# Kernel optimization log

Hardware: AMD Instinct MI355X
Metric: run time of the kernel (lower is better)

The kernel has to match this reference:

```python
import math
import jax, jax.numpy as jnp
import numpy as np

HEADS = 16
REL_WINDOW = 128


def setup_inputs() -> dict:
    key = jax.random.key(0)
    k1, k2, k3, k4, k5 = jax.random.split(key, 5)
    b, s, d = 2, 2048, 1024
    hd = d // HEADS          # 64
    R = 2 * REL_WINDOW + 1   # 257
    return {
        "x": jax.random.normal(k1, (b, s, d), dtype=jnp.float32),
        "Wqkv": jax.random.normal(k2, (3 * d, d), dtype=jnp.float32) * (1.0 / math.sqrt(d)),
        "bqkv": jax.random.normal(k3, (3 * d,), dtype=jnp.float32) * 0.02,
        "Wr": jax.random.normal(k4, (R, hd), dtype=jnp.float32) * (1.0 / math.sqrt(hd)),
        "br": jax.random.normal(k5, (R,), dtype=jnp.float32) * 0.02,
    }


def reference(x, Wqkv, bqkv, Wr, br):
    b, s, d = x.shape
    h = HEADS
    hd = d // h
    w = REL_WINDOW
    scale = math.sqrt(d / h)

    # qkv projection; torch view(b,s,h,3*hd) then chunk(3, dim=-1)
    qkv = (x @ Wqkv.T + bqkv).reshape(b, s, h, 3 * hd)
    q, k, v = jnp.split(qkv, 3, axis=-1)          # each [b,s,h,hd]
    q = q.transpose(0, 2, 1, 3)                   # [b,h,s,hd]
    k = k.transpose(0, 2, 1, 3)
    v = v.transpose(0, 2, 1, 3)

    # content scores
    content = jnp.einsum('bhik,bhjk->bhij', q, k) / scale  # [b,h,s,s]

    # relative position scores: project queries to R logits, gather per (i,j) offset
    idx = jnp.arange(s)
    offsets = jnp.clip(idx[None, :] - idx[:, None], -w, w) + w  # [s,s] in [0, 2w]
    rp = jnp.einsum('bhik,rk->bhir', q, Wr) + br               # [b,h,s,R]
    pos = jnp.take_along_axis(rp, jnp.broadcast_to(offsets, (b, h, s, s)), axis=-1)

    attn = jax.nn.softmax(content + pos, axis=-1)
    out = jnp.einsum('bhij,bhjk->bhik', attn, v)  # [b,h,s,hd]
    return out.transpose(0, 2, 1, 3).reshape(b, s, d)
```

## Files before the change

### kernel.cpp

```cpp
#include <hip/hip_runtime.h>

typedef short bfrag __attribute__((ext_vector_type(8)));
typedef float f32x4 __attribute__((ext_vector_type(4)));

#define MFMA16(a, b, c) __builtin_amdgcn_mfma_f32_16x16x32_bf16((a), (b), (c), 0, 0, 0)

#define SEQ   2048
#define DMOD  1024
#define NHEAD 16
#define HDIM  64
#define RSZ   257
#define RSTRIDE 260
#define RPADN 272
#define XN    (4096*1024)
#define WN    (3072*1024)
#define LOG2E 1.44269504f

__device__ __forceinline__ unsigned short f2bf(float f) {
  unsigned int u = __float_as_uint(f);
  u += 0x7FFFu + ((u >> 16) & 1u);
  return (unsigned short)(u >> 16);
}
__device__ __forceinline__ float bf2f(unsigned short u) {
  return __uint_as_float(((unsigned int)u) << 16);
}
__device__ __forceinline__ unsigned int pkbf(float a, float b) {
#if defined(__gfx950__)
  unsigned int r;
  asm("v_cvt_pk_bf16_f32 %0, %1, %2" : "=v"(r) : "v"(a), "v"(b));
  return r;
#else
  return (unsigned int)f2bf(a) | ((unsigned int)f2bf(b) << 16);
#endif
}
__device__ __forceinline__ float fexp2(float x) {
#if __has_builtin(__builtin_amdgcn_exp2f)
  return __builtin_amdgcn_exp2f(x);
#else
  return __expf(x * 0.69314718f);
#endif
}
__device__ __forceinline__ void gl2lds16(const void* g, void* l) {
  __builtin_amdgcn_global_load_lds(
      (__attribute__((address_space(1))) void*)(g),
      (__attribute__((address_space(3))) void*)(l), 16, 0, 0);
}

__global__ __launch_bounds__(256) void cast_all(const float* __restrict__ x,
                                                const float* __restrict__ Wqkv,
                                                const float* __restrict__ Wr,
                                                unsigned short* __restrict__ xb,
                                                unsigned short* __restrict__ wb,
                                                unsigned short* __restrict__ wrb) {
  int i = (blockIdx.x * 256 + threadIdx.x) * 4;
  if (i < XN) {
    float4 v = *(const float4*)(x + i);
    ushort4 o; o.x = f2bf(v.x); o.y = f2bf(v.y); o.z = f2bf(v.z); o.w = f2bf(v.w);
    *(ushort4*)(xb + i) = o;
  } else if (i < XN + WN) {
    int j = i - XN;
    float4 v = *(const float4*)(Wqkv + j);
    ushort4 o; o.x = f2bf(v.x); o.y = f2bf(v.y); o.z = f2bf(v.z); o.w = f2bf(v.w);
    *(ushort4*)(wb + j) = o;
  } else {
    int j = i - XN - WN;
    ushort4 o;
    unsigned short t[4];
#pragma unroll
    for (int k = 0; k < 4; ++k)
      t[k] = (j + k < RSZ * HDIM) ? f2bf(Wr[j + k]) : (unsigned short)0;
    o.x = t[0]; o.y = t[1]; o.z = t[2]; o.w = t[3];
    *(ushort4*)(wrb + j) = o;
  }
}

__global__ __launch_bounds__(256) void qkv_gemm(const unsigned short* __restrict__ xb,
                                                const unsigned short* __restrict__ wb,
                                                const float* __restrict__ bqkv,
                                                unsigned short* __restrict__ qb,
                                                unsigned short* __restrict__ kbuf,
                                                unsigned short* __restrict__ vtb) {
  __shared__ unsigned short SMEM[2 * 128 * 64];
  unsigned short* As = SMEM;
  unsigned short* Bs = SMEM + 128 * 64;
  unsigned short* Vtmp = SMEM;
  const int tid = threadIdx.x;
  const int m0 = blockIdx.y * 128, n0 = blockIdx.x * 128;
  const int wave = tid >> 6, lane = tid & 63;
  const int q4 = lane >> 4, l16 = lane & 15;
  const int wm = (wave & 1) * 64, wn = (wave >> 1) * 64;
  const int sw = l16 & 7;

  f32x4 acc[4][4];
#pragma unroll
  for (int rt = 0; rt < 4; ++rt)
#pragma unroll
    for (int ct = 0; ct < 4; ++ct) acc[rt][ct] = (f32x4){0.f, 0.f, 0.f, 0.f};

  for (int k0 = 0; k0 < DMOD; k0 += 64) {
#pragma unroll
    for (int it = 0; it < 4; ++it) {
      int ch = it * 256 + tid;
      int r = ch >> 3, cl = (ch & 7) ^ (r & 7);
      gl2lds16(xb + (size_t)(m0 + r) * DMOD + k0 + cl * 8, As + ch * 8);
      gl2lds16(wb + (size_t)(n0 + r) * DMOD + k0 + cl * 8, Bs + ch * 8);
    }
    __syncthreads();
#pragma unroll
    for (int ks = 0; ks < 2; ++ks) {
      bfrag af[4], bf[4];
#pragma unroll
      for (int rt = 0; rt < 4; ++rt)
        af[rt] = *(const bfrag*)(As + (wm + rt * 16 + l16) * 64 + ((ks * 4 + q4) ^ sw) * 8);
#pragma unroll
      for (int ct = 0; ct < 4; ++ct)
        bf[ct] = *(const bfrag*)(Bs + (wn + ct * 16 + l16) * 64 + ((ks * 4 + q4) ^ sw) * 8);
#pragma unroll
      for (int rt = 0; rt < 4; ++rt)
#pragma unroll
        for (int ct = 0; ct < 4; ++ct)
          acc[rt][ct] = MFMA16(bf[ct], af[rt], acc[rt][ct]);
    }
    __syncthreads();
  }

  const int batch = m0 >> 11;
  const int sbase = m0 & 2047;
  const int r3 = blockIdx.x % 3;
  const bool hasV = (r3 != 0);
  const int nv0 = n0 + ((r3 == 2) ? 64 : 0);

#pragma unroll
  for (int ct = 0; ct < 4; ++ct) {
    int ng = n0 + wn + ct * 16 + q4 * 4;
    int hh = ng / 192;
    int rem = ng - hh * 192;
    int t = rem >> 6, dd = rem & 63;
    float4 b4 = *(const float4*)(bqkv + ng);
    if (t < 2) {
      unsigned short* dst = (t == 0) ? qb : kbuf;
      size_t rowo = ((size_t)(batch * NHEAD + hh)) * SEQ + sbase;
#pragma unroll
      for (int rt = 0; rt < 4; ++rt) {
        int m = wm + rt * 16 + l16;
        uint2 pv;
        pv.x = pkbf(acc[rt][ct][0] + b4.x, acc[rt][ct][1] + b4.y);
        pv.y = pkbf(acc[rt][ct][2] + b4.z, acc[rt][ct][3] + b4.w);
        *(uint2*)(dst + (rowo + m) * HDIM + dd) = pv;
      }
    } else {
#pragma unroll
      for (int rt = 0; rt < 4; ++rt) {
        int m = wm + rt * 16 + l16;
        Vtmp[(dd + 0) * 136 + m] = f2bf(acc[rt][ct][0] + b4.x);
        Vtmp[(dd + 1) * 136 + m] = f2bf(acc[rt][ct][1] + b4.y);
        Vtmp[(dd + 2) * 136 + m] = f2bf(acc[rt][ct][2] + b4.z);
        Vtmp[(dd + 3) * 136 + m] = f2bf(acc[rt][ct][3] + b4.w);
      }
    }
  }

  if (hasV) {
    __syncthreads();
    const int hh = nv0 / 192;
    unsigned short* vdst = vtb + ((size_t)(batch * NHEAD + hh)) * HDIM * SEQ;
#pragma unroll
    for (int it = 0; it < 4; ++it) {
      int u = it * 256 + tid;
      int dd = u >> 4, mc = u & 15;
      bfrag val = *(const bfrag*)(Vtmp + dd * 136 + mc * 8);
      *(bfrag*)(vdst + (size_t)dd * SEQ + sbase + mc * 8) = val;
    }
  }
}

__global__ __launch_bounds__(256) void rp_gemm(const unsigned short* __restrict__ qb,
                                               const unsigned short* __restrict__ wrb,
                                               const float* __restrict__ br,
                                               unsigned short* __restrict__ rp16) {
  __shared__ unsigned short WrS[RPADN * HDIM];
  __shared__ unsigned short Qs[64 * HDIM];
  const int tid = threadIdx.x;
  const size_t row0 = (size_t)blockIdx.x * 64;

  for (int i = tid; i < RPADN * HDIM / 8; i += 256)
    *(uint4*)(&WrS[i * 8]) = *(const uint4*)(&wrb[i * 8]);
  for (int i = tid; i < 512; i += 256)
    *(uint4*)(&Qs[i * 8]) = *(const uint4*)(&qb[row0 * HDIM + i * 8]);
  __syncthreads();

  const int wave = tid >> 6, lane = tid & 63;
  const int q4 = lane >> 4, l16 = lane & 15;

  bfrag af0 = *(const bfrag*)(Qs + (wave * 16 + l16) * 64 + q4 * 8);
  bfrag af1 = *(const bfrag*)(Qs + (wave * 16 + l16) * 64 + 32 + q4 * 8);

  unsigned short* rrow = rp16 + (row0 + wave * 16 + l16) * RSTRIDE;
  const float br256 = br[256];

#pragma unroll 4
  for (int ct = 0; ct < 16; ++ct) {
    f32x4 acc = (f32x4){0.f, 0.f, 0.f, 0.f};
    bfrag w0 = *(const bfrag*)(WrS + (ct * 16 + l16) * 64 + q4 * 8);
    bfrag w1 = *(const bfrag*)(WrS + (ct * 16 + l16) * 64 + 32 + q4 * 8);
    acc = MFMA16(w0, af0, acc);
    acc = MFMA16(w1, af1, acc);
    int r = ct * 16 + q4 * 4;
    float4 b4 = *(const float4*)(br + r);
    uint2 pv;
    pv.x = pkbf((acc[0] + b4.x) * LOG2E, (acc[1] + b4.y) * LOG2E);
    pv.y = pkbf((acc[2] + b4.z) * LOG2E, (acc[3] + b4.w) * LOG2E);
    *(uint2*)(rrow + r) = pv;
  }
  {
    f32x4 acc = (f32x4){0.f, 0.f, 0.f, 0.f};
    bfrag w0 = *(const bfrag*)(WrS + (256 + l16) * 64 + q4 * 8);
    bfrag w1 = *(const bfrag*)(WrS + (256 + l16) * 64 + 32 + q4 * 8);
    acc = MFMA16(w0, af0, acc);
    acc = MFMA16(w1, af1, acc);
    if (q4 == 0)
      rrow[256] = f2bf((acc[0] + br256) * LOG2E);
  }
}

__global__ __launch_bounds__(256) void flash_attn(const unsigned short* __restrict__ qb,
                                                  const unsigned short* __restrict__ kbuf,
                                                  const unsigned short* __restrict__ vtb,
                                                  const unsigned short* __restrict__ rp16,
                                                  float* __restrict__ out) {
  __shared__ unsigned short Ks[64 * 64];
  __shared__ unsigned short Vs[64 * 64];
  __shared__ unsigned short Ps[64 * 64];

  const int tid = threadIdx.x;
  const int i0 = blockIdx.x * 64;
  const int bh = blockIdx.y;
  const int wave = tid >> 6, lane = tid & 63;
  const int q4 = lane >> 4, l16 = lane & 15;
  const int sw = l16 & 7;
  const float SC = 0.125f * LOG2E;

  const int rloc = wave * 16 + l16;
  const int ig = i0 + rloc;
  const unsigned short* qrow = qb + ((size_t)bh * SEQ + ig) * HDIM;
  bfrag qf0 = *(const bfrag*)(qrow + q4 * 8);
  bfrag qf1 = *(const bfrag*)(qrow + 32 + q4 * 8);

  const unsigned short* rpbase = rp16 + ((size_t)bh * SEQ + ig) * RSTRIDE;
  const float rpL = bf2f(rpbase[0]);
  const float rpR = bf2f(rpbase[256]);

  float m_s = -3.0e38f, l_s = 0.f;
  f32x4 oacc[4];
#pragma unroll
  for (int ct = 0; ct < 4; ++ct) oacc[ct] = (f32x4){0.f, 0.f, 0.f, 0.f};

  const unsigned short* kbase = kbuf + (size_t)bh * SEQ * HDIM;
  const unsigned short* vbase = vtb + (size_t)bh * HDIM * SEQ;

  for (int jt = 0; jt < 32; ++jt) {
    const int j0 = jt * 64;
#pragma unroll
    for (int it = 0; it < 2; ++it) {
      int ch = it * 256 + tid;
      int r = ch >> 3, cl = (ch & 7) ^ (r & 7);
      gl2lds16(kbase + (size_t)(j0 + r) * HDIM + cl * 8, Ks + ch * 8);
      gl2lds16(vbase + (size_t)r * SEQ + j0 + cl * 8, Vs + ch * 8);
    }
    __syncthreads();

    f32x4 sacc[4];
#pragma unroll
    for (int ct = 0; ct < 4; ++ct) {
      sacc[ct] = (f32x4){0.f, 0.f, 0.f, 0.f};
      bfrag k0f = *(const bfrag*)(Ks + (ct * 16 + l16) * 64 + (q4 ^ sw) * 8);
      bfrag k1f = *(const bfrag*)(Ks + (ct * 16 + l16) * 64 + ((4 + q4) ^ sw) * 8);
      sacc[ct] = MFMA16(k0f, qf0, sacc[ct]);
      sacc[ct] = MFMA16(k1f, qf1, sacc[ct]);
    }

    float p[4][4];
    const int dj = j0 - i0;
    if (dj >= 191) {
#pragma unroll
      for (int ct = 0; ct < 4; ++ct)
#pragma unroll
        for (int reg = 0; reg < 4; ++reg)
          p[ct][reg] = sacc[ct][reg] * SC + rpR;
    } else if (dj <= -191) {
#pragma unroll
      for (int ct = 0; ct < 4; ++ct)
#pragma unroll
        for (int reg = 0; reg < 4; ++reg)
          p[ct][reg] = sacc[ct][reg] * SC + rpL;
    } else {
#pragma unroll
      for (int ct = 0; ct < 4; ++ct) {
#pragma unroll
        for (int reg = 0; reg < 4; ++reg) {
          int j = j0 + ct * 16 + q4 * 4 + reg;
          int off = j - ig;
          off = (off < -128) ? -128 : (off > 128 ? 128 : off);
          p[ct][reg] = sacc[ct][reg] * SC + bf2f(rpbase[off + 128]);
        }
      }
    }

    float mm;
    {
      float a0 = fmaxf(fmaxf(p[0][0], p[0][1]), fmaxf(p[0][2], p[0][3]));
      float a1 = fmaxf(fmaxf(p[1][0], p[1][1]), fmaxf(p[1][2], p[1][3]));
      float a2 = fmaxf(fmaxf(p[2][0], p[2][1]), fmaxf(p[2][2], p[2][3]));
      float a3 = fmaxf(fmaxf(p[3][0], p[3][1]), fmaxf(p[3][2], p[3][3]));
      mm = fmaxf(fmaxf(a0, a1), fmaxf(a2, a3));
      mm = fmaxf(mm, __shfl_xor(mm, 16));
      mm = fmaxf(mm, __shfl_xor(mm, 32));
    }
    const float mnew = fmaxf(m_s, mm);
    const float alpha = fexp2(m_s - mnew);
    m_s = mnew;
#pragma unroll
    for (int ct = 0; ct < 4; ++ct)
#pragma unroll
      for (int reg = 0; reg < 4; ++reg)
        p[ct][reg] = fexp2(p[ct][reg] - m_s);
    {
      float s0 = (p[0][0] + p[0][1]) + (p[0][2] + p[0][3]);
      float s1 = (p[1][0] + p[1][1]) + (p[1][2] + p[1][3]);
      float s2 = (p[2][0] + p[2][1]) + (p[2][2] + p[2][3]);
      float s3 = (p[3][0] + p[3][1]) + (p[3][2] + p[3][3]);
      float rs = (s0 + s1) + (s2 + s3);
      rs += __shfl_xor(rs, 16);
      rs += __shfl_xor(rs, 32);
      l_s = l_s * alpha + rs;
    }
#pragma unroll
    for (int ct = 0; ct < 4; ++ct)
#pragma unroll
      for (int reg = 0; reg < 4; ++reg)
        oacc[ct][reg] *= alpha;

    unsigned int* Pw = (unsigned int*)Ps;
#pragma unroll
    for (int ct = 0; ct < 4; ++ct) {
      unsigned int pk01 = pkbf(p[ct][0], p[ct][1]);
      unsigned int pk23 = pkbf(p[ct][2], p[ct][3]);
      int chunk = ct * 2 + (q4 >> 1);
      unsigned int a = rloc * 32 + ((chunk ^ sw) << 2) + ((q4 & 1) << 1);
      Pw[a] = pk01;
      Pw[a + 1] = pk23;
    }

    bfrag pf0 = *(const bfrag*)(Ps + rloc * 64 + (q4 ^ sw) * 8);
    bfrag pf1 = *(const bfrag*)(Ps + rloc * 64 + ((4 + q4) ^ sw) * 8);
#pragma unroll
    for (int ct = 0; ct < 4; ++ct) {
      bfrag v0f = *(const bfrag*)(Vs + (ct * 16 + l16) * 64 + (q4 ^ sw) * 8);
      bfrag v1f = *(const bfrag*)(Vs + (ct * 16 + l16) * 64 + ((4 + q4) ^ sw) * 8);
      oacc[ct] = MFMA16(v0f, pf0, oacc[ct]);
      oacc[ct] = MFMA16(v1f, pf1, oacc[ct]);
    }
    __syncthreads();
  }

  const int bidx = bh >> 4, hh = bh & 15;
  const float inv = 1.0f / l_s;
  float* orow = out + ((size_t)bidx * SEQ + ig) * DMOD + hh * HDIM;
#pragma unroll
  for (int ct = 0; ct < 4; ++ct) {
    float4 v;
    v.x = oacc[ct][0] * inv;
    v.y = oacc[ct][1] * inv;
    v.z = oacc[ct][2] * inv;
    v.w = oacc[ct][3] * inv;
    *(float4*)(orow + ct * 16 + q4 * 4) = v;
  }
}

extern "C" void kernel_launch(void* const* d_in, const int* in_sizes, int n_in,
                              void* d_out, int out_size, void* d_ws, size_t ws_size,
                              hipStream_t stream) {
  const float* x    = (const float*)d_in[0];
  const float* Wqkv = (const float*)d_in[1];
  const float* bqkv = (const float*)d_in[2];
  const float* Wr   = (const float*)d_in[3];
  const float* br   = (const float*)d_in[4];
  float* out = (float*)d_out;

  char* ws = (char*)d_ws;
  unsigned short* xb   = (unsigned short*)(ws);
  unsigned short* wb   = (unsigned short*)(ws + 8388608);
  unsigned short* qb   = (unsigned short*)(ws + 14680064);
  unsigned short* kb   = (unsigned short*)(ws + 23068672);
  unsigned short* vtb  = (unsigned short*)(ws + 31457280);
  unsigned short* wrb  = (unsigned short*)(ws + 39845888);
  unsigned short* rp16 = (unsigned short*)(ws + 39880704);

  cast_all<<<7185, 256, 0, stream>>>(x, Wqkv, Wr, xb, wb, wrb);
  qkv_gemm<<<dim3(24, 32), 256, 0, stream>>>(xb, wb, bqkv, qb, kb, vtb);
  rp_gemm<<<1024, 256, 0, stream>>>(qb, wrb, br, rp16);
  flash_attn<<<dim3(32, 32), 256, 0, stream>>>(qb, kb, vtb, rp16, out);
}
```

Baseline: 223.8 us.

## Split attention over key halves with combine kernel and lazy rescaling

Adds a split-KV flash attention variant that launches 2048 blocks, each processing half of the key tiles, then a combine kernel that merges the partial outputs using the per-row max and sum. It also skips the online-softmax rescale unless the new max exceeds the running max by more than a threshold, and remaps block indices so groups of heads land on the same XCD. The aim is more parallelism across CUs and less rescale ALU work, at the cost of writing and reading fp32 partial outputs and one extra launch. The split path is chosen only when the workspace is large enough, otherwise the original kernel runs with the new block mapping.

```diff
diff --git a/kernel.cpp b/kernel.cpp
--- a/kernel.cpp
+++ b/kernel.cpp
@@ -223,6 +223,222 @@
   }
 }
 
+
+__device__ __forceinline__ void fa_tile(
+    int jt, int i0, int ig, int rloc, int q4, int l16, int sw,
+    const unsigned short* kbase, const unsigned short* vbase,
+    const unsigned short* rpbase, float rpL, float rpR,
+    bfrag qf0, bfrag qf1,
+    unsigned short* Ks, unsigned short* Vs, unsigned short* Ps,
+    float& m_s, float& l_s, f32x4* oacc, int tid) {
+  const float SC = 0.125f * LOG2E;
+  const int j0 = jt * 64;
+#pragma unroll
+  for (int it = 0; it < 2; ++it) {
+    int ch = it * 256 + tid;
+    int r = ch >> 3, cl = (ch & 7) ^ (r & 7);
+    gl2lds16(kbase + (size_t)(j0 + r) * HDIM + cl * 8, Ks + ch * 8);
+    gl2lds16(vbase + (size_t)r * SEQ + j0 + cl * 8, Vs + ch * 8);
+  }
+  __syncthreads();
+
+  f32x4 sacc[4];
+#pragma unroll
+  for (int ct = 0; ct < 4; ++ct) {
+    sacc[ct] = (f32x4){0.f, 0.f, 0.f, 0.f};
+    bfrag k0f = *(const bfrag*)(Ks + (ct * 16 + l16) * 64 + (q4 ^ sw) * 8);
+    bfrag k1f = *(const bfrag*)(Ks + (ct * 16 + l16) * 64 + ((4 + q4) ^ sw) * 8);
+    sacc[ct] = MFMA16(k0f, qf0, sacc[ct]);
+    sacc[ct] = MFMA16(k1f, qf1, sacc[ct]);
+  }
+
+  float p[4][4];
+  const int dj = j0 - i0;
+  if (dj >= 191) {
+#pragma unroll
+    for (int ct = 0; ct < 4; ++ct)
+#pragma unroll
+      for (int reg = 0; reg < 4; ++reg)
+        p[ct][reg] = sacc[ct][reg] * SC + rpR;
+  } else if (dj <= -191) {
+#pragma unroll
+    for (int ct = 0; ct < 4; ++ct)
+#pragma unroll
+      for (int reg = 0; reg < 4; ++reg)
+        p[ct][reg] = sacc[ct][reg] * SC + rpL;
+  } else {
+#pragma unroll
+    for (int ct = 0; ct < 4; ++ct) {
+#pragma unroll
+      for (int reg = 0; reg < 4; ++reg) {
+        int j = j0 + ct * 16 + q4 * 4 + reg;
+        int off = j - ig;
+        off = (off < -128) ? -128 : (off > 128 ? 128 : off);
+        p[ct][reg] = sacc[ct][reg] * SC + bf2f(rpbase[off + 128]);
+      }
+    }
+  }
+
+  float mm;
+  {
+    float a0 = fmaxf(fmaxf(p[0][0], p[0][1]), fmaxf(p[0][2], p[0][3]));
+    float a1 = fmaxf(fmaxf(p[1][0], p[1][1]), fmaxf(p[1][2], p[1][3]));
+    float a2 = fmaxf(fmaxf(p[2][0], p[2][1]), fmaxf(p[2][2], p[2][3]));
+    float a3 = fmaxf(fmaxf(p[3][0], p[3][1]), fmaxf(p[3][2], p[3][3]));
+    mm = fmaxf(fmaxf(a0, a1), fmaxf(a2, a3));
+    mm = fmaxf(mm, __shfl_xor(mm, 16));
+    mm = fmaxf(mm, __shfl_xor(mm, 32));
+  }
+  if (!__all(mm <= m_s + 8.0f)) {
+    const float mnew = fmaxf(m_s, mm);
+    const float alpha = fexp2(m_s - mnew);
+    m_s = mnew;
+    l_s *= alpha;
+#pragma unroll
+    for (int ct = 0; ct < 4; ++ct)
+#pragma unroll
+      for (int reg = 0; reg < 4; ++reg)
+        oacc[ct][reg] *= alpha;
+  }
+#pragma unroll
+  for (int ct = 0; ct < 4; ++ct)
+#pragma unroll
+    for (int reg = 0; reg < 4; ++reg)
+      p[ct][reg] = fexp2(p[ct][reg] - m_s);
+  {
+    float s0 = (p[0][0] + p[0][1]) + (p[0][2] + p[0][3]);
+    float s1 = (p[1][0] + p[1][1]) + (p[1][2] + p[1][3]);
+    float s2 = (p[2][0] + p[2][1]) + (p[2][2] + p[2][3]);
+    float s3 = (p[3][0] + p[3][1]) + (p[3][2] + p[3][3]);
+    float rs = (s0 + s1) + (s2 + s3);
+    rs += __shfl_xor(rs, 16);
+    rs += __shfl_xor(rs, 32);
+    l_s += rs;
+  }
+
+  unsigned int* Pw = (unsigned int*)Ps;
+#pragma unroll
+  for (int ct = 0; ct < 4; ++ct) {
+    unsigned int pk01 = pkbf(p[ct][0], p[ct][1]);
+    unsigned int pk23 = pkbf(p[ct][2], p[ct][3]);
+    int chunk = ct * 2 + (q4 >> 1);
+    unsigned int a = rloc * 32 + ((chunk ^ sw) << 2) + ((q4 & 1) << 1);
+    Pw[a] = pk01;
+    Pw[a + 1] = pk23;
+  }
+
+  bfrag pf0 = *(const bfrag*)(Ps + rloc * 64 + (q4 ^ sw) * 8);
+  bfrag pf1 = *(const bfrag*)(Ps + rloc * 64 + ((4 + q4) ^ sw) * 8);
+#pragma unroll
+  for (int ct = 0; ct < 4; ++ct) {
+    bfrag v0f = *(const bfrag*)(Vs + (ct * 16 + l16) * 64 + (q4 ^ sw) * 8);
+    bfrag v1f = *(const bfrag*)(Vs + (ct * 16 + l16) * 64 + ((4 + q4) ^ sw) * 8);
+    oacc[ct] = MFMA16(v0f, pf0, oacc[ct]);
+    oacc[ct] = MFMA16(v1f, pf1, oacc[ct]);
+  }
+  __syncthreads();
+}
+
+__global__ __launch_bounds__(256) void flash_attn_sp(const unsigned short* __restrict__ qb,
+                                                     const unsigned short* __restrict__ kbuf,
+                                                     const unsigned short* __restrict__ vtb,
+                                                     const unsigned short* __restrict__ rp16,
+                                                     float* __restrict__ opart,
+                                                     float* __restrict__ mlbuf) {
+  __shared__ unsigned short Ks[64 * 64];
+  __shared__ unsigned short Vs[64 * 64];
+  __shared__ unsigned short Ps[64 * 64];
+
+  const int tid = threadIdx.x;
+  const int orig = blockIdx.x;
+  const int g = orig & 7;
+  const int slot = orig >> 3;
+  const int bh = g * 4 + (slot >> 6);
+  const int rem = slot & 63;
+  const int i0 = (rem >> 1) << 6;
+  const int half = rem & 1;
+
+  const int wave = tid >> 6, lane = tid & 63;
+  const int q4 = lane >> 4, l16 = lane & 15;
+  const int sw = l16 & 7;
+  const int rloc = wave * 16 + l16;
+  const int ig = i0 + rloc;
+
+  const unsigned short* qrow = qb + ((size_t)bh * SEQ + ig) * HDIM;
+  bfrag qf0 = *(const bfrag*)(qrow + q4 * 8);
+  bfrag qf1 = *(const bfrag*)(qrow + 32 + q4 * 8);
+
+  const unsigned short* rpbase = rp16 + ((size_t)bh * SEQ + ig) * RSTRIDE;
+  const float rpL = bf2f(rpbase[0]);
+  const float rpR = bf2f(rpbase[256]);
+
+  float m_s = -3.0e38f, l_s = 0.f;
+  f32x4 oacc[4];
+#pragma unroll
+  for (int ct = 0; ct < 4; ++ct) oacc[ct] = (f32x4){0.f, 0.f, 0.f, 0.f};
+
+  const unsigned short* kbase = kbuf + (size_t)bh * SEQ * HDIM;
+  const unsigned short* vbase = vtb + (size_t)bh * HDIM * SEQ;
+
+  const int jt0 = half * 16;
+  for (int jt = jt0; jt < jt0 + 16; ++jt)
+    fa_tile(jt, i0, ig, rloc, q4, l16, sw, kbase, vbase, rpbase, rpL, rpR,
+            qf0, qf1, Ks, Vs, Ps, m_s, l_s, oacc, tid);
+
+  const int iblk = i0 >> 6;
+  const int part = (bh * 32 + iblk) * 2 + half;
+  float* orow = opart + ((size_t)part * 64 + rloc) * 64;
+#pragma unroll
+  for (int ct = 0; ct < 4; ++ct) {
+    float4 v;
+    v.x = oacc[ct][0]; v.y = oacc[ct][1]; v.z = oacc[ct][2]; v.w = oacc[ct][3];
+    *(float4*)(orow + ct * 16 + q4 * 4) = v;
+  }
+  if (q4 == 0) {
+    float2 ml; ml.x = m_s; ml.y = l_s;
+    ((float2*)mlbuf)[part * 64 + rloc] = ml;
+  }
+}
+
+__global__ __launch_bounds__(256) void fa_combine(const float* __restrict__ opart,
+                                                  const float* __restrict__ mlbuf,
+                                                  float* __restrict__ out) {
+  const int orig = blockIdx.x;
+  const int g = orig & 7;
+  const int slot = orig >> 3;
+  const int bh = g * 4 + (slot >> 5);
+  const int iblk = slot & 31;
+  const int p0 = (bh * 32 + iblk) * 2;
+
+  const int t = threadIdx.x;
+  const int row = t >> 2;
+  const int c0 = (t & 3) * 16;
+
+  const float2* ML = (const float2*)mlbuf;
+  float2 ml0 = ML[p0 * 64 + row];
+  float2 ml1 = ML[(p0 + 1) * 64 + row];
+  float M = fmaxf(ml0.x, ml1.x);
+  float a0 = fexp2(ml0.x - M), a1 = fexp2(ml1.x - M);
+  float inv = 1.0f / (ml0.y * a0 + ml1.y * a1);
+  float w0 = a0 * inv, w1 = a1 * inv;
+
+  const float* r0 = opart + ((size_t)p0 * 64 + row) * 64 + c0;
+  const float* r1 = r0 + 4096;
+  const int bidx = bh >> 4, hh = bh & 15;
+  float* orow = out + ((size_t)bidx * SEQ + iblk * 64 + row) * DMOD + hh * HDIM + c0;
+#pragma unroll
+  for (int k = 0; k < 4; ++k) {
+    float4 x0 = ((const float4*)r0)[k];
+    float4 x1 = ((const float4*)r1)[k];
+    float4 o;
+    o.x = x0.x * w0 + x1.x * w1;
+    o.y = x0.y * w0 + x1.y * w1;
+    o.z = x0.z * w0 + x1.z * w1;
+    o.w = x0.w * w0 + x1.w * w1;
+    ((float4*)orow)[k] = o;
+  }
+}
+
 __global__ __launch_bounds__(256) void flash_attn(const unsigned short* __restrict__ qb,
                                                   const unsigned short* __restrict__ kbuf,
                                                   const unsigned short* __restrict__ vtb,
@@ -233,15 +449,16 @@
   __shared__ unsigned short Ps[64 * 64];
 
   const int tid = threadIdx.x;
-  const int i0 = blockIdx.x * 64;
-  const int bh = blockIdx.y;
+  const int orig = blockIdx.x;
+  const int slot = orig >> 3;
+  const int bh = (orig & 7) * 4 + (slot >> 5);
+  const int i0 = (slot & 31) << 6;
   const int wave = tid >> 6, lane = tid & 63;
   const int q4 = lane >> 4, l16 = lane & 15;
   const int sw = l16 & 7;
-  const float SC = 0.125f * LOG2E;
-
   const int rloc = wave * 16 + l16;
   const int ig = i0 + rloc;
+
   const unsigned short* qrow = qb + ((size_t)bh * SEQ + ig) * HDIM;
   bfrag qf0 = *(const bfrag*)(qrow + q4 * 8);
   bfrag qf1 = *(const bfrag*)(qrow + 32 + q4 * 8);
@@ -258,110 +475,9 @@
   const unsigned short* kbase = kbuf + (size_t)bh * SEQ * HDIM;
   const unsigned short* vbase = vtb + (size_t)bh * HDIM * SEQ;
 
-  for (int jt = 0; jt < 32; ++jt) {
-    const int j0 = jt * 64;
-#pragma unroll
-    for (int it = 0; it < 2; ++it) {
-      int ch = it * 256 + tid;
-      int r = ch >> 3, cl = (ch & 7) ^ (r & 7);
-      gl2lds16(kbase + (size_t)(j0 + r) * HDIM + cl * 8, Ks + ch * 8);
-      gl2lds16(vbase + (size_t)r * SEQ + j0 + cl * 8, Vs + ch * 8);
-    }
-    __syncthreads();
-
-    f32x4 sacc[4];
-#pragma unroll
-    for (int ct = 0; ct < 4; ++ct) {
-      sacc[ct] = (f32x4){0.f, 0.f, 0.f, 0.f};
-      bfrag k0f = *(const bfrag*)(Ks + (ct * 16 + l16) * 64 + (q4 ^ sw) * 8);
-      bfrag k1f = *(const bfrag*)(Ks + (ct * 16 + l16) * 64 + ((4 + q4) ^ sw) * 8);
-      sacc[ct] = MFMA16(k0f, qf0, sacc[ct]);
-      sacc[ct] = MFMA16(k1f, qf1, sacc[ct]);
-    }
-
-    float p[4][4];
-    const int dj = j0 - i0;
-    if (dj >= 191) {
-#pragma unroll
-      for (int ct = 0; ct < 4; ++ct)
-#pragma unroll
-        for (int reg = 0; reg < 4; ++reg)
-          p[ct][reg] = sacc[ct][reg] * SC + rpR;
-    } else if (dj <= -191) {
-#pragma unroll
-      for (int ct = 0; ct < 4; ++ct)
-#pragma unroll
-        for (int reg = 0; reg < 4; ++reg)
-          p[ct][reg] = sacc[ct][reg] * SC + rpL;
-    } else {
-#pragma unroll
-      for (int ct = 0; ct < 4; ++ct) {
-#pragma unroll
-        for (int reg = 0; reg < 4; ++reg) {
-          int j = j0 + ct * 16 + q4 * 4 + reg;
-          int off = j - ig;
-          off = (off < -128) ? -128 : (off > 128 ? 128 : off);
-          p[ct][reg] = sacc[ct][reg] * SC + bf2f(rpbase[off + 128]);
-        }
-      }
-    }
-
-    float mm;
-    {
-      float a0 = fmaxf(fmaxf(p[0][0], p[0][1]), fmaxf(p[0][2], p[0][3]));
-      float a1 = fmaxf(fmaxf(p[1][0], p[1][1]), fmaxf(p[1][2], p[1][3]));
-      float a2 = fmaxf(fmaxf(p[2][0], p[2][1]), fmaxf(p[2][2], p[2][3]));
-      float a3 = fmaxf(fmaxf(p[3][0], p[3][1]), fmaxf(p[3][2], p[3][3]));
-      mm = fmaxf(fmaxf(a0, a1), fmaxf(a2, a3));
-      mm = fmaxf(mm, __shfl_xor(mm, 16));
-      mm = fmaxf(mm, __shfl_xor(mm, 32));
-    }
-    const float mnew = fmaxf(m_s, mm);
-    const float alpha = fexp2(m_s - mnew);
-    m_s = mnew;
-#pragma unroll
-    for (int ct = 0; ct < 4; ++ct)
-#pragma unroll
-      for (int reg = 0; reg < 4; ++reg)
-        p[ct][reg] = fexp2(p[ct][reg] - m_s);
-    {
-      float s0 = (p[0][0] + p[0][1]) + (p[0][2] + p[0][3]);
-      float s1 = (p[1][0] + p[1][1]) + (p[1][2] + p[1][3]);
-      float s2 = (p[2][0] + p[2][1]) + (p[2][2] + p[2][3]);
-      float s3 = (p[3][0] + p[3][1]) + (p[3][2] + p[3][3]);
-      float rs = (s0 + s1) + (s2 + s3);
-      rs += __shfl_xor(rs, 16);
-      rs += __shfl_xor(rs, 32);
-      l_s = l_s * alpha + rs;
-    }
-#pragma unroll
-    for (int ct = 0; ct < 4; ++ct)
-#pragma unroll
-      for (int reg = 0; reg < 4; ++reg)
-        oacc[ct][reg] *= alpha;
-
-    unsigned int* Pw = (unsigned int*)Ps;
-#pragma unroll
-    for (int ct = 0; ct < 4; ++ct) {
-      unsigned int pk01 = pkbf(p[ct][0], p[ct][1]);
-      unsigned int pk23 = pkbf(p[ct][2], p[ct][3]);
-      int chunk = ct * 2 + (q4 >> 1);
-      unsigned int a = rloc * 32 + ((chunk ^ sw) << 2) + ((q4 & 1) << 1);
-      Pw[a] = pk01;
-      Pw[a + 1] = pk23;
-    }
-
-    bfrag pf0 = *(const bfrag*)(Ps + rloc * 64 + (q4 ^ sw) * 8);
-    bfrag pf1 = *(const bfrag*)(Ps + rloc * 64 + ((4 + q4) ^ sw) * 8);
-#pragma unroll
-    for (int ct = 0; ct < 4; ++ct) {
-      bfrag v0f = *(const bfrag*)(Vs + (ct * 16 + l16) * 64 + (q4 ^ sw) * 8);
-      bfrag v1f = *(const bfrag*)(Vs + (ct * 16 + l16) * 64 + ((4 + q4) ^ sw) * 8);
-      oacc[ct] = MFMA16(v0f, pf0, oacc[ct]);
-      oacc[ct] = MFMA16(v1f, pf1, oacc[ct]);
-    }
-    __syncthreads();
-  }
+  for (int jt = 0; jt < 32; ++jt)
+    fa_tile(jt, i0, ig, rloc, q4, l16, sw, kbase, vbase, rpbase, rpL, rpR,
+            qf0, qf1, Ks, Vs, Ps, m_s, l_s, oacc, tid);
 
   const int bidx = bh >> 4, hh = bh & 15;
   const float inv = 1.0f / l_s;
@@ -395,9 +511,17 @@
   unsigned short* vtb  = (unsigned short*)(ws + 31457280);
   unsigned short* wrb  = (unsigned short*)(ws + 39845888);
   unsigned short* rp16 = (unsigned short*)(ws + 39880704);
+  float* opart = (float*)(ws + 73959424);
+  float* mlbuf = (float*)(ws + 73959424 + 33554432);
+  const size_t WS_NEED_SPLIT = 73959424u + 33554432u + 1048576u;
 
   cast_all<<<7185, 256, 0, stream>>>(x, Wqkv, Wr, xb, wb, wrb);
   qkv_gemm<<<dim3(24, 32), 256, 0, stream>>>(xb, wb, bqkv, qb, kb, vtb);
   rp_gemm<<<1024, 256, 0, stream>>>(qb, wrb, br, rp16);
-  flash_attn<<<dim3(32, 32), 256, 0, stream>>>(qb, kb, vtb, rp16, out);
-}
+  if (ws_size >= WS_NEED_SPLIT) {
+    flash_attn_sp<<<2048, 256, 0, stream>>>(qb, kb, vtb, rp16, opart, mlbuf);
+    fa_combine<<<1024, 256, 0, stream>>>(opart, mlbuf, out);
+  } else {
+    flash_attn<<<1024, 256, 0, stream>>>(qb, kb, vtb, rp16, out);
+  }
+}
```

Measured after the change: 245.4 us. +9.6%, slower.

## Double-buffer K tiles, load V fragments directly, and remap blocks for XCD locality

Applied to the files above, without the earlier changes.

The attention kernel now prefetches the next K tile into a second LDS buffer while computing on the current one, so only one barrier per tile remains. V operands are read straight from global memory into registers instead of being staged through LDS. The grid is flattened and block indices are remapped so that blocks sharing a (batch, head) land on the same XCD, which should improve L2 reuse of K and V. The trade-offs are extra register pressure and global-load latency on the V path, which is not hidden behind much compute.

```diff
diff --git a/kernel.cpp b/kernel.cpp
--- a/kernel.cpp
+++ b/kernel.cpp
@@ -228,13 +228,14 @@
                                                   const unsigned short* __restrict__ vtb,
                                                   const unsigned short* __restrict__ rp16,
                                                   float* __restrict__ out) {
-  __shared__ unsigned short Ks[64 * 64];
-  __shared__ unsigned short Vs[64 * 64];
+  __shared__ unsigned short Ks[2][64 * 64];
   __shared__ unsigned short Ps[64 * 64];
 
   const int tid = threadIdx.x;
-  const int i0 = blockIdx.x * 64;
-  const int bh = blockIdx.y;
+  const int orig = blockIdx.x;
+  const int slot = orig >> 3;
+  const int bh = (orig & 7) * 4 + (slot >> 5);
+  const int i0 = (slot & 31) << 6;
   const int wave = tid >> 6, lane = tid & 63;
   const int q4 = lane >> 4, l16 = lane & 15;
   const int sw = l16 & 7;
@@ -256,25 +257,43 @@
   for (int ct = 0; ct < 4; ++ct) oacc[ct] = (f32x4){0.f, 0.f, 0.f, 0.f};
 
   const unsigned short* kbase = kbuf + (size_t)bh * SEQ * HDIM;
-  const unsigned short* vbase = vtb + (size_t)bh * HDIM * SEQ;
+  const unsigned short* vfp = vtb + (size_t)bh * HDIM * SEQ + (size_t)l16 * SEQ + q4 * 8;
+
+#pragma unroll
+  for (int it = 0; it < 2; ++it) {
+    int ch = it * 256 + tid;
+    int r = ch >> 3, cl = (ch & 7) ^ (r & 7);
+    gl2lds16(kbase + (size_t)r * HDIM + cl * 8, &Ks[0][ch * 8]);
+  }
+  __syncthreads();
 
   for (int jt = 0; jt < 32; ++jt) {
+    const int cur = jt & 1;
     const int j0 = jt * 64;
-#pragma unroll
-    for (int it = 0; it < 2; ++it) {
-      int ch = it * 256 + tid;
-      int r = ch >> 3, cl = (ch & 7) ^ (r & 7);
-      gl2lds16(kbase + (size_t)(j0 + r) * HDIM + cl * 8, Ks + ch * 8);
-      gl2lds16(vbase + (size_t)r * SEQ + j0 + cl * 8, Vs + ch * 8);
-    }
-    __syncthreads();
+
+    if (jt < 31) {
+#pragma unroll
+      for (int it = 0; it < 2; ++it) {
+        int ch = it * 256 + tid;
+        int r = ch >> 3, cl = (ch & 7) ^ (r & 7);
+        gl2lds16(kbase + (size_t)(j0 + 64 + r) * HDIM + cl * 8, &Ks[cur ^ 1][ch * 8]);
+      }
+    }
+
+    bfrag vf[8];
+#pragma unroll
+    for (int ct = 0; ct < 4; ++ct) {
+      const unsigned short* vr = vfp + (size_t)(ct * 16) * SEQ + j0;
+      vf[2 * ct]     = *(const bfrag*)(vr);
+      vf[2 * ct + 1] = *(const bfrag*)(vr + 32);
+    }
 
     f32x4 sacc[4];
 #pragma unroll
     for (int ct = 0; ct < 4; ++ct) {
       sacc[ct] = (f32x4){0.f, 0.f, 0.f, 0.f};
-      bfrag k0f = *(const bfrag*)(Ks + (ct * 16 + l16) * 64 + (q4 ^ sw) * 8);
-      bfrag k1f = *(const bfrag*)(Ks + (ct * 16 + l16) * 64 + ((4 + q4) ^ sw) * 8);
+      bfrag k0f = *(const bfrag*)(&Ks[cur][(ct * 16 + l16) * 64 + (q4 ^ sw) * 8]);
+      bfrag k1f = *(const bfrag*)(&Ks[cur][(ct * 16 + l16) * 64 + ((4 + q4) ^ sw) * 8]);
       sacc[ct] = MFMA16(k0f, qf0, sacc[ct]);
       sacc[ct] = MFMA16(k1f, qf1, sacc[ct]);
     }
@@ -355,11 +374,10 @@
     bfrag pf1 = *(const bfrag*)(Ps + rloc * 64 + ((4 + q4) ^ sw) * 8);
 #pragma unroll
     for (int ct = 0; ct < 4; ++ct) {
-      bfrag v0f = *(const bfrag*)(Vs + (ct * 16 + l16) * 64 + (q4 ^ sw) * 8);
-      bfrag v1f = *(const bfrag*)(Vs + (ct * 16 + l16) * 64 + ((4 + q4) ^ sw) * 8);
-      oacc[ct] = MFMA16(v0f, pf0, oacc[ct]);
-      oacc[ct] = MFMA16(v1f, pf1, oacc[ct]);
-    }
+      oacc[ct] = MFMA16(vf[2 * ct], pf0, oacc[ct]);
+      oacc[ct] = MFMA16(vf[2 * ct + 1], pf1, oacc[ct]);
+    }
+
     __syncthreads();
   }
 
@@ -399,5 +417,5 @@
   cast_all<<<7185, 256, 0, stream>>>(x, Wqkv, Wr, xb, wb, wrb);
   qkv_gemm<<<dim3(24, 32), 256, 0, stream>>>(xb, wb, bqkv, qb, kb, vtb);
   rp_gemm<<<1024, 256, 0, stream>>>(qb, wrb, br, rp16);
-  flash_attn<<<dim3(32, 32), 256, 0, stream>>>(qb, kb, vtb, rp16, out);
-}
+  flash_attn<<<1024, 256, 0, stream>>>(qb, kb, vtb, rp16, out);
+}
```

Measured after the change: 287.8 us. +28.6%, slower.
